# Kernel optimization log

Measured on AMD Instinct MI355X. Metric: run time of the kernel, lower is better.

The kernel has to match this reference:

```python
import jax, jax.numpy as jnp
import numpy as np

N_NODES = 50000
N_EDGES = 500000
IN_DIM = 128
HIDDEN = 32
HEADS = 8
OUT_DIM = HIDDEN * HEADS  # 256
NEG_SLOPE = 0.2


def setup_inputs() -> dict:
    key = jax.random.key(0)
    ks = jax.random.split(key, 10)
    s = lambda fan: 1.0 / np.sqrt(fan)
    x = jax.random.normal(ks[0], (N_NODES, IN_DIM), dtype=jnp.float32)
    edge_index = jax.random.randint(ks[1], (2, N_EDGES), 0, N_NODES, dtype=jnp.int32)
    W1 = jax.random.normal(ks[2], (IN_DIM, HEADS * HIDDEN), jnp.float32) * s(IN_DIM)
    a_src1 = jax.random.normal(ks[3], (HEADS, HIDDEN), jnp.float32) * s(HIDDEN)
    a_dst1 = jax.random.normal(ks[4], (HEADS, HIDDEN), jnp.float32) * s(HIDDEN)
    b1 = jnp.zeros((HEADS * HIDDEN,), jnp.float32)
    W2 = jax.random.normal(ks[5], (OUT_DIM, OUT_DIM), jnp.float32) * s(OUT_DIM)
    a_src2 = jax.random.normal(ks[6], (1, OUT_DIM), jnp.float32) * s(OUT_DIM)
    a_dst2 = jax.random.normal(ks[7], (1, OUT_DIM), jnp.float32) * s(OUT_DIM)
    b2 = jnp.zeros((OUT_DIM,), jnp.float32)
    return {"x": x, "edge_index": edge_index, "W1": W1, "a_src1": a_src1,
            "a_dst1": a_dst1, "b1": b1, "W2": W2, "a_src2": a_src2,
            "a_dst2": a_dst2, "b2": b2}


def _gat_layer(x, src, dst, W, a_src, a_dst, b, heads, ch, concat):
    N = x.shape[0]
    h = (x @ W).reshape(N, heads, ch)                      # [N,H,C]
    e_src = jnp.sum(h * a_src[None], axis=-1)              # [N,H]
    e_dst = jnp.sum(h * a_dst[None], axis=-1)              # [N,H]
    e = jax.nn.leaky_relu(e_src[src] + e_dst[dst], NEG_SLOPE)  # [E,H]
    # softmax over incoming edges of each destination node
    m = jax.ops.segment_max(e, dst, num_segments=N)        # [N,H]
    e = jnp.exp(e - m[dst])
    denom = jax.ops.segment_sum(e, dst, num_segments=N)    # [N,H]
    alpha = e / (denom[dst] + 1e-16)                       # [E,H]
    msg = h[src] * alpha[:, :, None]                       # [E,H,C]
    out = jax.ops.segment_sum(msg, dst, num_segments=N)    # [N,H,C]
    out = out.reshape(N, heads * ch) if concat else out.mean(axis=1)
    return out + b


def reference(x, edge_index, W1, a_src1, a_dst1, b1, W2, a_src2, a_dst2, b2):
    N = x.shape[0]
    # add self loops (PyG GATConv default)
    loops = jnp.arange(N, dtype=edge_index.dtype)
    src = jnp.concatenate([edge_index[0], loops])
    dst = jnp.concatenate([edge_index[1], loops])
    # dropout is identity in eval mode
    h = _gat_layer(x, src, dst, W1, a_src1, a_dst1, b1, HEADS, HIDDEN, True)
    h = jax.nn.elu(h)
    out = _gat_layer(h, src, dst, W2, a_src2, a_dst2, b2, 1, OUT_DIM, False)
    return out
```

## Files before the change

### kernel.cpp

```cpp
#include <hip/hip_runtime.h>
#include <math.h>

#define N_NODES 50000
#define E_ORIG  500000
#define E_TOT   550000
#define NB      196
#define AGG_GB  1563

typedef _Float16 half8  __attribute__((ext_vector_type(8)));
typedef _Float16 half4  __attribute__((ext_vector_type(4)));
typedef float    v4f    __attribute__((ext_vector_type(4)));
typedef int      int4u  __attribute__((ext_vector_type(4), aligned(4)));

__global__ void k_prepw(const float* __restrict__ W1, const float* __restrict__ W2,
                        const float* __restrict__ as2, const float* __restrict__ ad2,
                        const int* __restrict__ ei,
                        _Float16* __restrict__ w1t, _Float16* __restrict__ w2t,
                        float* __restrict__ vs2, float* __restrict__ vd2,
                        int* __restrict__ deg) {
    int i = blockIdx.x * blockDim.x + threadIdx.x;
    if (i < E_TOT) {
        int d = (i < E_ORIG) ? ei[E_ORIG + i] : (i - E_ORIG);
        atomicAdd(&deg[d], 1);
        return;
    }
    int j = i - E_TOT;
    if (j < 128 * 256) {
        int k = j >> 8, c = j & 255;
        w1t[(size_t)c * 128 + k] = (_Float16)W1[j];
        return;
    }
    j -= 128 * 256;
    if (j < 256 * 256) {
        int k = j >> 8, c = j & 255;
        w2t[(size_t)c * 256 + k] = (_Float16)W2[j];
        return;
    }
    j -= 256 * 256;
    if (j < 256) {
        float s = 0.f, d = 0.f;
        for (int c = 0; c < 256; c++) {
            float w = W2[(size_t)j * 256 + c];
            s += w * as2[c];
            d += w * ad2[c];
        }
        vs2[j] = s;
        vd2[j] = d;
    }
}

__global__ __launch_bounds__(256) void k_blocksum(const int* __restrict__ deg,
                                                  int* __restrict__ bsum) {
    int t = threadIdx.x;
    int i = blockIdx.x * 256 + t;
    int v = (i < N_NODES) ? deg[i] : 0;
#pragma unroll
    for (int mk = 1; mk < 64; mk <<= 1) v += __shfl_xor(v, mk, 64);
    __shared__ int ws[4];
    if ((t & 63) == 0) ws[t >> 6] = v;
    __syncthreads();
    if (t == 0) bsum[blockIdx.x] = ws[0] + ws[1] + ws[2] + ws[3];
}

__global__ __launch_bounds__(256) void k_scanbsum(const int* __restrict__ bsum,
                                                  int* __restrict__ boff) {
    __shared__ int s[256];
    int t = threadIdx.x;
    int v = (t < NB) ? bsum[t] : 0;
    s[t] = v;
    __syncthreads();
    for (int o = 1; o < 256; o <<= 1) {
        int x = (t >= o) ? s[t - o] : 0;
        __syncthreads();
        s[t] += x;
        __syncthreads();
    }
    if (t <= NB) boff[t] = (t == 0) ? 0 : s[t - 1];
}

__global__ __launch_bounds__(256) void k_offsets(const int* __restrict__ deg,
                                                 const int* __restrict__ boff,
                                                 int* __restrict__ offsets,
                                                 int* __restrict__ cur) {
    __shared__ int s[256];
    int t = threadIdx.x;
    int i = blockIdx.x * 256 + t;
    int v = (i < N_NODES) ? deg[i] : 0;
    s[t] = v;
    __syncthreads();
    for (int o = 1; o < 256; o <<= 1) {
        int x = (t >= o) ? s[t - o] : 0;
        __syncthreads();
        s[t] += x;
        __syncthreads();
    }
    int off = boff[blockIdx.x] + s[t] - v;
    if (i <= N_NODES) {
        offsets[i] = off;
        if (i < N_NODES) cur[i] = off;
    }
}

__global__ void k_scatter(const int* __restrict__ ei, int* __restrict__ cur,
                          int* __restrict__ csr_src) {
    int e = blockIdx.x * blockDim.x + threadIdx.x;
    if (e >= E_TOT) return;
    int s, d;
    if (e < E_ORIG) { s = ei[e]; d = ei[E_ORIG + e]; }
    else            { s = e - E_ORIG; d = s; }
    int slot = atomicAdd(&cur[d], 1);
    csr_src[slot] = s;
}

__global__ __launch_bounds__(256) void k_gemm1(
    const float* __restrict__ X, const _Float16* __restrict__ Bt,
    const float* __restrict__ a_s, const float* __restrict__ a_d,
    _Float16* __restrict__ H, float* __restrict__ es, float* __restrict__ ed) {
    int t = threadIdx.x, w = t >> 6, lane = t & 63;
    int quad = lane >> 4, l16 = lane & 15;
    int row0 = blockIdx.x * 32;
    int colbase = w * 64;

    v4f acc[2][4];
#pragma unroll
    for (int i = 0; i < 2; i++)
#pragma unroll
        for (int j = 0; j < 4; j++) acc[i][j] = (v4f){0.f, 0.f, 0.f, 0.f};

    int r0 = row0 + l16;      if (r0 >= N_NODES) r0 = N_NODES - 1;
    int r1 = row0 + 16 + l16; if (r1 >= N_NODES) r1 = N_NODES - 1;
    const float4* a0p = (const float4*)(X + (size_t)r0 * 128) + quad * 2;
    const float4* a1p = (const float4*)(X + (size_t)r1 * 128) + quad * 2;
    const half8* bp[4];
#pragma unroll
    for (int ct = 0; ct < 4; ct++)
        bp[ct] = (const half8*)(Bt + (size_t)(colbase + ct * 16 + l16) * 128 + quad * 8);

#pragma unroll
    for (int kc = 0; kc < 4; kc++) {
        float4 f0 = a0p[kc * 8], f1 = a0p[kc * 8 + 1];
        float4 f2 = a1p[kc * 8], f3 = a1p[kc * 8 + 1];
        half8 av0 = (half8){(_Float16)f0.x, (_Float16)f0.y, (_Float16)f0.z, (_Float16)f0.w,
                            (_Float16)f1.x, (_Float16)f1.y, (_Float16)f1.z, (_Float16)f1.w};
        half8 av1 = (half8){(_Float16)f2.x, (_Float16)f2.y, (_Float16)f2.z, (_Float16)f2.w,
                            (_Float16)f3.x, (_Float16)f3.y, (_Float16)f3.z, (_Float16)f3.w};
#pragma unroll
        for (int ct = 0; ct < 4; ct++) {
            half8 bv = bp[ct][kc * 4];
            acc[0][ct] = __builtin_amdgcn_mfma_f32_16x16x32_f16(av0, bv, acc[0][ct], 0, 0, 0);
            acc[1][ct] = __builtin_amdgcn_mfma_f32_16x16x32_f16(av1, bv, acc[1][ct], 0, 0, 0);
        }
    }

    float asv[4], adv[4];
#pragma unroll
    for (int ct = 0; ct < 4; ct++) {
        asv[ct] = a_s[colbase + ct * 16 + l16];
        adv[ct] = a_d[colbase + ct * 16 + l16];
    }
#pragma unroll
    for (int rt = 0; rt < 2; rt++) {
#pragma unroll
        for (int hp = 0; hp < 2; hp++) {
#pragma unroll
            for (int reg = 0; reg < 4; reg++) {
                float ps = acc[rt][2 * hp][reg] * asv[2 * hp] +
                           acc[rt][2 * hp + 1][reg] * asv[2 * hp + 1];
                float pd = acc[rt][2 * hp][reg] * adv[2 * hp] +
                           acc[rt][2 * hp + 1][reg] * adv[2 * hp + 1];
#pragma unroll
                for (int mk = 1; mk < 16; mk <<= 1) {
                    ps += __shfl_xor(ps, mk, 64);
                    pd += __shfl_xor(pd, mk, 64);
                }
                if (l16 == 0) {
                    int row = row0 + rt * 16 + quad * 4 + reg;
                    if (row < N_NODES) {
                        int head = w * 2 + hp;
                        es[(size_t)head * N_NODES + row] = ps;
                        ed[(size_t)head * N_NODES + row] = pd;
                    }
                }
            }
        }
    }

    __shared__ _Float16 SH[16][264];
#pragma unroll
    for (int rt = 0; rt < 2; rt++) {
        if (rt) __syncthreads();
#pragma unroll
        for (int ct = 0; ct < 4; ct++)
#pragma unroll
            for (int reg = 0; reg < 4; reg++)
                SH[quad * 4 + reg][colbase + ct * 16 + l16] = (_Float16)acc[rt][ct][reg];
        __syncthreads();
#pragma unroll
        for (int j = 0; j < 2; j++) {
            int c = j * 256 + t;
            int row = c >> 5, col8 = c & 31;
            int gr = row0 + rt * 16 + row;
            if (gr < N_NODES) {
                int head = col8 >> 2, sub = col8 & 3;
                *(half8*)(H + ((size_t)head * N_NODES + gr) * 32 + sub * 8) =
                    *(const half8*)&SH[row][col8 * 8];
            }
        }
    }
}

__global__ __launch_bounds__(256) void k_gemm2(
    const _Float16* __restrict__ A, const _Float16* __restrict__ Bt,
    const float* __restrict__ bias, float* __restrict__ OUT) {
    int t = threadIdx.x, w = t >> 6, lane = t & 63;
    int quad = lane >> 4, l16 = lane & 15;
    int row0 = blockIdx.x * 32;
    int colbase = w * 64;

    v4f acc[2][4];
#pragma unroll
    for (int i = 0; i < 2; i++)
#pragma unroll
        for (int j = 0; j < 4; j++) acc[i][j] = (v4f){0.f, 0.f, 0.f, 0.f};

    int r0 = row0 + l16;      if (r0 >= N_NODES) r0 = N_NODES - 1;
    int r1 = row0 + 16 + l16; if (r1 >= N_NODES) r1 = N_NODES - 1;
    const half8* a0 = (const half8*)(A + (size_t)r0 * 256 + quad * 8);
    const half8* a1 = (const half8*)(A + (size_t)r1 * 256 + quad * 8);
    const half8* bp[4];
#pragma unroll
    for (int ct = 0; ct < 4; ct++)
        bp[ct] = (const half8*)(Bt + (size_t)(colbase + ct * 16 + l16) * 256 + quad * 8);

#pragma unroll
    for (int kc = 0; kc < 8; kc++) {
        half8 av0 = a0[kc * 4];
        half8 av1 = a1[kc * 4];
#pragma unroll
        for (int ct = 0; ct < 4; ct++) {
            half8 bv = bp[ct][kc * 4];
            acc[0][ct] = __builtin_amdgcn_mfma_f32_16x16x32_f16(av0, bv, acc[0][ct], 0, 0, 0);
            acc[1][ct] = __builtin_amdgcn_mfma_f32_16x16x32_f16(av1, bv, acc[1][ct], 0, 0, 0);
        }
    }

    __shared__ float SF[16][260];
#pragma unroll
    for (int rt = 0; rt < 2; rt++) {
        if (rt) __syncthreads();
#pragma unroll
        for (int ct = 0; ct < 4; ct++)
#pragma unroll
            for (int reg = 0; reg < 4; reg++)
                SF[quad * 4 + reg][colbase + ct * 16 + l16] = acc[rt][ct][reg];
        __syncthreads();
#pragma unroll
        for (int j = 0; j < 4; j++) {
            int c = j * 256 + t;
            int row = c >> 6, c4 = c & 63;
            int gr = row0 + rt * 16 + row;
            if (gr < N_NODES) {
                float4 v = *(const float4*)&SF[row][c4 * 4];
                float4 bb = ((const float4*)bias)[c4];
                float4 o = make_float4(v.x + bb.x, v.y + bb.y, v.z + bb.z, v.w + bb.w);
                *(float4*)(OUT + (size_t)gr * 256 + c4 * 4) = o;
            }
        }
    }
}

__global__ __launch_bounds__(256) void k_agg1(
    const _Float16* __restrict__ Hs, const float* __restrict__ esh,
    const float* __restrict__ edh, const int* __restrict__ offsets,
    const int* __restrict__ csr_src, const float* __restrict__ b1,
    const float* __restrict__ vs2, const float* __restrict__ vd2,
    _Float16* __restrict__ out1s, float* __restrict__ es2,
    float* __restrict__ ed2) {
    int t = threadIdx.x, w = t >> 6, lane = t & 63;
    int h  = blockIdx.x & 7;
    int gb = blockIdx.x >> 3;
    int g  = lane >> 3;
    int c4 = lane & 7;
    int nn = gb * 32 + w * 8 + g;
    bool valid = nn < N_NODES;
    int n = valid ? nn : N_NODES - 1;

    int beg = offsets[n];
    int deg = offsets[n + 1] - beg;
    float edn = edh[(size_t)h * N_NODES + n];

    const _Float16* __restrict__ Hb  = Hs + (size_t)h * N_NODES * 32;
    const float* __restrict__    esb = esh + (size_t)h * N_NODES;
    const int* __restrict__      sb  = csr_src + beg;
    int bpbase = (lane & 56) << 2;

    float a0 = 0.f, a1 = 0.f, a2 = 0.f, a3 = 0.f, den = 0.f;
    for (int base = 0; base < deg; base += 8) {
        int4u sv0 = *(const int4u*)(sb + base);
        int4u sv1 = *(const int4u*)(sb + base + 4);
        int s_mine = sb[base + c4];
        float l = esb[s_mine] + edn;
        l = fmaxf(l, 0.2f * l);
        float wm = (base + c4 < deg) ? __expf(l) : 0.f;
        den += wm;
        int wmi = __float_as_int(wm);
        half4 hv[8];
        hv[0] = *(const half4*)(Hb + (size_t)sv0[0] * 32 + c4 * 4);
        hv[1] = *(const half4*)(Hb + (size_t)sv0[1] * 32 + c4 * 4);
        hv[2] = *(const half4*)(Hb + (size_t)sv0[2] * 32 + c4 * 4);
        hv[3] = *(const half4*)(Hb + (size_t)sv0[3] * 32 + c4 * 4);
        hv[4] = *(const half4*)(Hb + (size_t)sv1[0] * 32 + c4 * 4);
        hv[5] = *(const half4*)(Hb + (size_t)sv1[1] * 32 + c4 * 4);
        hv[6] = *(const half4*)(Hb + (size_t)sv1[2] * 32 + c4 * 4);
        hv[7] = *(const half4*)(Hb + (size_t)sv1[3] * 32 + c4 * 4);
#pragma unroll
        for (int j = 0; j < 8; j++) {
            float wj = __int_as_float(
                __builtin_amdgcn_ds_bpermute(bpbase + 4 * j, wmi));
            a0 += wj * (float)hv[j][0]; a1 += wj * (float)hv[j][1];
            a2 += wj * (float)hv[j][2]; a3 += wj * (float)hv[j][3];
        }
    }
#pragma unroll
    for (int mk = 1; mk < 8; mk <<= 1) den += __shfl_xor(den, mk, 64);

    float r = 1.f / (den + 1e-16f);
    int c = h * 32 + c4 * 4;
    float4 bb = *(const float4*)(b1 + c);
    float o0 = a0 * r + bb.x, o1 = a1 * r + bb.y;
    float o2 = a2 * r + bb.z, o3 = a3 * r + bb.w;
    o0 = o0 > 0.f ? o0 : __expf(o0) - 1.f;
    o1 = o1 > 0.f ? o1 : __expf(o1) - 1.f;
    o2 = o2 > 0.f ? o2 : __expf(o2) - 1.f;
    o3 = o3 > 0.f ? o3 : __expf(o3) - 1.f;
    *(half4*)(out1s + ((size_t)h * N_NODES + n) * 32 + c4 * 4) =
        (half4){(_Float16)o0, (_Float16)o1, (_Float16)o2, (_Float16)o3};

    float4 vs = *(const float4*)(vs2 + c);
    float4 vd = *(const float4*)(vd2 + c);
    float ps = o0 * vs.x + o1 * vs.y + o2 * vs.z + o3 * vs.w;
    float pd = o0 * vd.x + o1 * vd.y + o2 * vd.z + o3 * vd.w;
#pragma unroll
    for (int mk = 1; mk < 8; mk <<= 1) {
        ps += __shfl_xor(ps, mk, 64);
        pd += __shfl_xor(pd, mk, 64);
    }
    if (c4 == 0 && valid) {
        atomicAdd(&es2[n], ps);
        atomicAdd(&ed2[n], pd);
    }
}

__global__ __launch_bounds__(256) void k_agg2(
    const _Float16* __restrict__ O1s, const float* __restrict__ es2,
    const float* __restrict__ ed2, const int* __restrict__ offsets,
    const int* __restrict__ csr_src, _Float16* __restrict__ xagg) {
    int t = threadIdx.x, w = t >> 6, lane = t & 63;
    int h  = blockIdx.x & 7;
    int gb = blockIdx.x >> 3;
    int g  = lane >> 3;
    int c4 = lane & 7;
    int nn = gb * 32 + w * 8 + g;
    bool valid = nn < N_NODES;
    int n = valid ? nn : N_NODES - 1;

    int beg = offsets[n];
    int deg = offsets[n + 1] - beg;
    float edn = ed2[n];

    const _Float16* __restrict__ Ob = O1s + (size_t)h * N_NODES * 32;
    const int* __restrict__     sb  = csr_src + beg;
    int bpbase = (lane & 56) << 2;

    float a0 = 0.f, a1 = 0.f, a2 = 0.f, a3 = 0.f, den = 0.f;
    for (int base = 0; base < deg; base += 8) {
        int4u sv0 = *(const int4u*)(sb + base);
        int4u sv1 = *(const int4u*)(sb + base + 4);
        int s_mine = sb[base + c4];
        float l = es2[s_mine] + edn;
        l = fmaxf(l, 0.2f * l);
        float wm = (base + c4 < deg) ? __expf(l) : 0.f;
        den += wm;
        int wmi = __float_as_int(wm);
        half4 hv[8];
        hv[0] = *(const half4*)(Ob + (size_t)sv0[0] * 32 + c4 * 4);
        hv[1] = *(const half4*)(Ob + (size_t)sv0[1] * 32 + c4 * 4);
        hv[2] = *(const half4*)(Ob + (size_t)sv0[2] * 32 + c4 * 4);
        hv[3] = *(const half4*)(Ob + (size_t)sv0[3] * 32 + c4 * 4);
        hv[4] = *(const half4*)(Ob + (size_t)sv1[0] * 32 + c4 * 4);
        hv[5] = *(const half4*)(Ob + (size_t)sv1[1] * 32 + c4 * 4);
        hv[6] = *(const half4*)(Ob + (size_t)sv1[2] * 32 + c4 * 4);
        hv[7] = *(const half4*)(Ob + (size_t)sv1[3] * 32 + c4 * 4);
#pragma unroll
        for (int j = 0; j < 8; j++) {
            float wj = __int_as_float(
                __builtin_amdgcn_ds_bpermute(bpbase + 4 * j, wmi));
            a0 += wj * (float)hv[j][0]; a1 += wj * (float)hv[j][1];
            a2 += wj * (float)hv[j][2]; a3 += wj * (float)hv[j][3];
        }
    }
#pragma unroll
    for (int mk = 1; mk < 8; mk <<= 1) den += __shfl_xor(den, mk, 64);

    float r = 1.f / (den + 1e-16f);
    *(half4*)(xagg + (size_t)n * 256 + h * 32 + c4 * 4) =
        (half4){(_Float16)(a0 * r), (_Float16)(a1 * r),
                (_Float16)(a2 * r), (_Float16)(a3 * r)};
}

extern "C" void kernel_launch(void* const* d_in, const int* in_sizes, int n_in,
                              void* d_out, int out_size, void* d_ws, size_t ws_size,
                              hipStream_t stream) {
    const float* x   = (const float*)d_in[0];
    const int*   ei  = (const int*)d_in[1];
    const float* W1  = (const float*)d_in[2];
    const float* as1 = (const float*)d_in[3];
    const float* ad1 = (const float*)d_in[4];
    const float* b1  = (const float*)d_in[5];
    const float* W2  = (const float*)d_in[6];
    const float* as2 = (const float*)d_in[7];
    const float* ad2 = (const float*)d_in[8];
    const float* b2  = (const float*)d_in[9];
    float* out = (float*)d_out;

    char* ws = (char*)d_ws;
    size_t off = 0;
    auto alloc = [&](size_t bytes) {
        void* p = ws + off;
        off = (off + bytes + 255) & ~(size_t)255;
        return p;
    };
    _Float16* h1h     = (_Float16*)alloc((size_t)N_NODES * 256 * 2);
    _Float16* out1h   = (_Float16*)alloc((size_t)N_NODES * 256 * 2);
    _Float16* xagg    = (_Float16*)alloc((size_t)N_NODES * 256 * 2);
    _Float16* w1t     = (_Float16*)alloc((size_t)128 * 256 * 2);
    _Float16* w2t     = (_Float16*)alloc((size_t)256 * 256 * 2);
    float*    es1     = (float*)alloc((size_t)N_NODES * 8 * 4);
    float*    ed1     = (float*)alloc((size_t)N_NODES * 8 * 4);
    float*    es2     = (float*)alloc((size_t)N_NODES * 4);
    float*    ed2     = (float*)alloc((size_t)N_NODES * 4);
    float*    vs2     = (float*)alloc(256 * 4);
    float*    vd2     = (float*)alloc(256 * 4);
    int*      deg     = (int*)alloc((size_t)N_NODES * 4);
    int*      offsets = (int*)alloc((size_t)(N_NODES + 1) * 4);
    int*      cur     = (int*)alloc((size_t)N_NODES * 4);
    int*      csr_src = (int*)alloc((size_t)(E_TOT + 8) * 4);
    int*      bsum    = (int*)alloc((size_t)NB * 4);
    int*      boff    = (int*)alloc((size_t)(NB + 1) * 4);

    const int TB = 256;
    int gridE = (E_TOT + TB - 1) / TB;
    int gridG = (N_NODES + 31) / 32;
    int gridA = AGG_GB * 8;

    hipMemsetAsync(deg, 0, (size_t)N_NODES * 4, stream);
    hipMemsetAsync(es2, 0, (size_t)N_NODES * 4, stream);
    hipMemsetAsync(ed2, 0, (size_t)N_NODES * 4, stream);
    hipMemsetAsync(csr_src + E_TOT, 0, 8 * 4, stream);
    int prepN = E_TOT + 128 * 256 + 256 * 256 + 256;
    k_prepw<<<(prepN + TB - 1) / TB, TB, 0, stream>>>(W1, W2, as2, ad2, ei,
                                                      w1t, w2t, vs2, vd2, deg);
    k_blocksum<<<NB, TB, 0, stream>>>(deg, bsum);
    k_scanbsum<<<1, TB, 0, stream>>>(bsum, boff);
    k_offsets<<<NB, TB, 0, stream>>>(deg, boff, offsets, cur);
    k_scatter<<<gridE, TB, 0, stream>>>(ei, cur, csr_src);

    k_gemm1<<<gridG, TB, 0, stream>>>(x, w1t, as1, ad1, h1h, es1, ed1);
    k_agg1<<<gridA, TB, 0, stream>>>(h1h, es1, ed1, offsets, csr_src, b1,
                                     vs2, vd2, out1h, es2, ed2);

    k_agg2<<<gridA, TB, 0, stream>>>(out1h, es2, ed2, offsets, csr_src, xagg);
    k_gemm2<<<gridG, TB, 0, stream>>>(xagg, w2t, b2, out);
}
```

Baseline: 371.2 us.

## Sort nodes by degree and use 4-lane groups with half8 gathers in aggregation

Adds a counting sort of nodes by in-degree (histogram, scan, rank) to build a permutation. The aggregation kernels walk that permutation, so nodes with similar degree share a wavefront and divergence is reduced. Each node now gets 4 lanes loading half8 instead of 8 lanes loading half4, processing 4 edges per iteration and doubling the nodes per wave. The cost is three extra small kernel launches, an extra perm load, and less coalesced output writes because neighbouring lanes now handle scattered nodes.

```diff
diff --git a/kernel.cpp b/kernel.cpp
--- a/kernel.cpp
+++ b/kernel.cpp
@@ -5,7 +5,7 @@
 #define E_ORIG  500000
 #define E_TOT   550000
 #define NB      196
-#define AGG_GB  1563
+#define AGG_GB  782
 
 typedef _Float16 half8  __attribute__((ext_vector_type(8)));
 typedef _Float16 half4  __attribute__((ext_vector_type(4)));
@@ -112,6 +112,39 @@
     csr_src[slot] = s;
 }
 
+__global__ __launch_bounds__(256) void k_hist(const int* __restrict__ deg,
+                                              int* __restrict__ hist) {
+    int i = blockIdx.x * 256 + threadIdx.x;
+    if (i < N_NODES) {
+        int b = deg[i]; if (b > 63) b = 63;
+        atomicAdd(&hist[b], 1);
+    }
+}
+
+__global__ __launch_bounds__(64) void k_scanhist(const int* __restrict__ hist,
+                                                 int* __restrict__ hcur) {
+    int t = threadIdx.x;
+    int v = hist[t];
+    int inc = v;
+#pragma unroll
+    for (int o = 1; o < 64; o <<= 1) {
+        int x = __shfl_up(inc, o, 64);
+        if (t >= o) inc += x;
+    }
+    hcur[t] = inc - v;
+}
+
+__global__ __launch_bounds__(256) void k_rank(const int* __restrict__ deg,
+                                              int* __restrict__ hcur,
+                                              int* __restrict__ perm) {
+    int i = blockIdx.x * 256 + threadIdx.x;
+    if (i < N_NODES) {
+        int b = deg[i]; if (b > 63) b = 63;
+        int r = atomicAdd(&hcur[b], 1);
+        perm[r] = i;
+    }
+}
+
 __global__ __launch_bounds__(256) void k_gemm1(
     const float* __restrict__ X, const _Float16* __restrict__ Bt,
     const float* __restrict__ a_s, const float* __restrict__ a_d,
@@ -272,18 +305,19 @@
 __global__ __launch_bounds__(256) void k_agg1(
     const _Float16* __restrict__ Hs, const float* __restrict__ esh,
     const float* __restrict__ edh, const int* __restrict__ offsets,
-    const int* __restrict__ csr_src, const float* __restrict__ b1,
-    const float* __restrict__ vs2, const float* __restrict__ vd2,
-    _Float16* __restrict__ out1s, float* __restrict__ es2,
-    float* __restrict__ ed2) {
+    const int* __restrict__ csr_src, const int* __restrict__ perm,
+    const float* __restrict__ b1, const float* __restrict__ vs2,
+    const float* __restrict__ vd2, _Float16* __restrict__ out1s,
+    float* __restrict__ es2, float* __restrict__ ed2) {
     int t = threadIdx.x, w = t >> 6, lane = t & 63;
     int h  = blockIdx.x & 7;
     int gb = blockIdx.x >> 3;
-    int g  = lane >> 3;
-    int c4 = lane & 7;
-    int nn = gb * 32 + w * 8 + g;
+    int g  = lane >> 2;
+    int l3 = lane & 3;
+    int nn = gb * 64 + w * 16 + g;
     bool valid = nn < N_NODES;
-    int n = valid ? nn : N_NODES - 1;
+    int rank = valid ? nn : N_NODES - 1;
+    int n = perm[rank];
 
     int beg = offsets[n];
     int deg = offsets[n + 1] - beg;
@@ -292,60 +326,68 @@
     const _Float16* __restrict__ Hb  = Hs + (size_t)h * N_NODES * 32;
     const float* __restrict__    esb = esh + (size_t)h * N_NODES;
     const int* __restrict__      sb  = csr_src + beg;
-    int bpbase = (lane & 56) << 2;
-
-    float a0 = 0.f, a1 = 0.f, a2 = 0.f, a3 = 0.f, den = 0.f;
-    for (int base = 0; base < deg; base += 8) {
-        int4u sv0 = *(const int4u*)(sb + base);
-        int4u sv1 = *(const int4u*)(sb + base + 4);
-        int s_mine = sb[base + c4];
-        float l = esb[s_mine] + edn;
+    int bp0 = (lane & 60) << 2;
+
+    float a[8] = {0.f, 0.f, 0.f, 0.f, 0.f, 0.f, 0.f, 0.f};
+    float den = 0.f;
+    for (int base = 0; base < deg; base += 4) {
+        int4u sv = *(const int4u*)(sb + base);
+        int sm = sv[0];
+        sm = (l3 == 1) ? sv[1] : sm;
+        sm = (l3 == 2) ? sv[2] : sm;
+        sm = (l3 == 3) ? sv[3] : sm;
+        float l = esb[sm] + edn;
         l = fmaxf(l, 0.2f * l);
-        float wm = (base + c4 < deg) ? __expf(l) : 0.f;
+        float wm = (base + l3 < deg) ? __expf(l) : 0.f;
         den += wm;
         int wmi = __float_as_int(wm);
-        half4 hv[8];
-        hv[0] = *(const half4*)(Hb + (size_t)sv0[0] * 32 + c4 * 4);
-        hv[1] = *(const half4*)(Hb + (size_t)sv0[1] * 32 + c4 * 4);
-        hv[2] = *(const half4*)(Hb + (size_t)sv0[2] * 32 + c4 * 4);
-        hv[3] = *(const half4*)(Hb + (size_t)sv0[3] * 32 + c4 * 4);
-        hv[4] = *(const half4*)(Hb + (size_t)sv1[0] * 32 + c4 * 4);
-        hv[5] = *(const half4*)(Hb + (size_t)sv1[1] * 32 + c4 * 4);
-        hv[6] = *(const half4*)(Hb + (size_t)sv1[2] * 32 + c4 * 4);
-        hv[7] = *(const half4*)(Hb + (size_t)sv1[3] * 32 + c4 * 4);
-#pragma unroll
-        for (int j = 0; j < 8; j++) {
-            float wj = __int_as_float(
-                __builtin_amdgcn_ds_bpermute(bpbase + 4 * j, wmi));
-            a0 += wj * (float)hv[j][0]; a1 += wj * (float)hv[j][1];
-            a2 += wj * (float)hv[j][2]; a3 += wj * (float)hv[j][3];
-        }
-    }
-#pragma unroll
-    for (int mk = 1; mk < 8; mk <<= 1) den += __shfl_xor(den, mk, 64);
+        half8 hv0 = *(const half8*)(Hb + (size_t)sv[0] * 32 + l3 * 8);
+        half8 hv1 = *(const half8*)(Hb + (size_t)sv[1] * 32 + l3 * 8);
+        half8 hv2 = *(const half8*)(Hb + (size_t)sv[2] * 32 + l3 * 8);
+        half8 hv3 = *(const half8*)(Hb + (size_t)sv[3] * 32 + l3 * 8);
+        float w0 = __int_as_float(__builtin_amdgcn_ds_bpermute(bp0,      wmi));
+        float w1 = __int_as_float(__builtin_amdgcn_ds_bpermute(bp0 + 4,  wmi));
+        float w2 = __int_as_float(__builtin_amdgcn_ds_bpermute(bp0 + 8,  wmi));
+        float w3 = __int_as_float(__builtin_amdgcn_ds_bpermute(bp0 + 12, wmi));
+#pragma unroll
+        for (int k = 0; k < 8; k++) {
+            a[k] += w0 * (float)hv0[k];
+            a[k] += w1 * (float)hv1[k];
+            a[k] += w2 * (float)hv2[k];
+            a[k] += w3 * (float)hv3[k];
+        }
+    }
+    den += __shfl_xor(den, 1, 64);
+    den += __shfl_xor(den, 2, 64);
 
     float r = 1.f / (den + 1e-16f);
-    int c = h * 32 + c4 * 4;
-    float4 bb = *(const float4*)(b1 + c);
-    float o0 = a0 * r + bb.x, o1 = a1 * r + bb.y;
-    float o2 = a2 * r + bb.z, o3 = a3 * r + bb.w;
-    o0 = o0 > 0.f ? o0 : __expf(o0) - 1.f;
-    o1 = o1 > 0.f ? o1 : __expf(o1) - 1.f;
-    o2 = o2 > 0.f ? o2 : __expf(o2) - 1.f;
-    o3 = o3 > 0.f ? o3 : __expf(o3) - 1.f;
-    *(half4*)(out1s + ((size_t)h * N_NODES + n) * 32 + c4 * 4) =
-        (half4){(_Float16)o0, (_Float16)o1, (_Float16)o2, (_Float16)o3};
-
-    float4 vs = *(const float4*)(vs2 + c);
-    float4 vd = *(const float4*)(vd2 + c);
-    float ps = o0 * vs.x + o1 * vs.y + o2 * vs.z + o3 * vs.w;
-    float pd = o0 * vd.x + o1 * vd.y + o2 * vd.z + o3 * vd.w;
-#pragma unroll
-    for (int mk = 1; mk < 8; mk <<= 1) {
-        ps += __shfl_xor(ps, mk, 64);
-        pd += __shfl_xor(pd, mk, 64);
-    }
-    if (c4 == 0 && valid) {
+    int c = h * 32 + l3 * 8;
+    float4 b0 = *(const float4*)(b1 + c);
+    float4 b4 = *(const float4*)(b1 + c + 4);
+    float o[8];
+    o[0] = a[0] * r + b0.x; o[1] = a[1] * r + b0.y;
+    o[2] = a[2] * r + b0.z; o[3] = a[3] * r + b0.w;
+    o[4] = a[4] * r + b4.x; o[5] = a[5] * r + b4.y;
+    o[6] = a[6] * r + b4.z; o[7] = a[7] * r + b4.w;
+    half8 ov;
+#pragma unroll
+    for (int k = 0; k < 8; k++) {
+        o[k] = o[k] > 0.f ? o[k] : __expf(o[k]) - 1.f;
+        ov[k] = (_Float16)o[k];
+    }
+    *(half8*)(out1s + ((size_t)h * N_NODES + n) * 32 + l3 * 8) = ov;
+
+    float4 vsa = *(const float4*)(vs2 + c);
+    float4 vsb = *(const float4*)(vs2 + c + 4);
+    float4 vda = *(const float4*)(vd2 + c);
+    float4 vdb = *(const float4*)(vd2 + c + 4);
+    float ps = o[0] * vsa.x + o[1] * vsa.y + o[2] * vsa.z + o[3] * vsa.w +
+               o[4] * vsb.x + o[5] * vsb.y + o[6] * vsb.z + o[7] * vsb.w;
+    float pd = o[0] * vda.x + o[1] * vda.y + o[2] * vda.z + o[3] * vda.w +
+               o[4] * vdb.x + o[5] * vdb.y + o[6] * vdb.z + o[7] * vdb.w;
+    ps += __shfl_xor(ps, 1, 64); ps += __shfl_xor(ps, 2, 64);
+    pd += __shfl_xor(pd, 1, 64); pd += __shfl_xor(pd, 2, 64);
+    if (l3 == 0 && valid) {
         atomicAdd(&es2[n], ps);
         atomicAdd(&ed2[n], pd);
     }
@@ -354,15 +396,17 @@
 __global__ __launch_bounds__(256) void k_agg2(
     const _Float16* __restrict__ O1s, const float* __restrict__ es2,
     const float* __restrict__ ed2, const int* __restrict__ offsets,
-    const int* __restrict__ csr_src, _Float16* __restrict__ xagg) {
+    const int* __restrict__ csr_src, const int* __restrict__ perm,
+    _Float16* __restrict__ xagg) {
     int t = threadIdx.x, w = t >> 6, lane = t & 63;
     int h  = blockIdx.x & 7;
     int gb = blockIdx.x >> 3;
-    int g  = lane >> 3;
-    int c4 = lane & 7;
-    int nn = gb * 32 + w * 8 + g;
+    int g  = lane >> 2;
+    int l3 = lane & 3;
+    int nn = gb * 64 + w * 16 + g;
     bool valid = nn < N_NODES;
-    int n = valid ? nn : N_NODES - 1;
+    int rank = valid ? nn : N_NODES - 1;
+    int n = perm[rank];
 
     int beg = offsets[n];
     int deg = offsets[n + 1] - beg;
@@ -370,42 +414,45 @@
 
     const _Float16* __restrict__ Ob = O1s + (size_t)h * N_NODES * 32;
     const int* __restrict__     sb  = csr_src + beg;
-    int bpbase = (lane & 56) << 2;
-
-    float a0 = 0.f, a1 = 0.f, a2 = 0.f, a3 = 0.f, den = 0.f;
-    for (int base = 0; base < deg; base += 8) {
-        int4u sv0 = *(const int4u*)(sb + base);
-        int4u sv1 = *(const int4u*)(sb + base + 4);
-        int s_mine = sb[base + c4];
-        float l = es2[s_mine] + edn;
+    int bp0 = (lane & 60) << 2;
+
+    float a[8] = {0.f, 0.f, 0.f, 0.f, 0.f, 0.f, 0.f, 0.f};
+    float den = 0.f;
+    for (int base = 0; base < deg; base += 4) {
+        int4u sv = *(const int4u*)(sb + base);
+        int sm = sv[0];
+        sm = (l3 == 1) ? sv[1] : sm;
+        sm = (l3 == 2) ? sv[2] : sm;
+        sm = (l3 == 3) ? sv[3] : sm;
+        float l = es2[sm] + edn;
         l = fmaxf(l, 0.2f * l);
-        float wm = (base + c4 < deg) ? __expf(l) : 0.f;
+        float wm = (base + l3 < deg) ? __expf(l) : 0.f;
         den += wm;
         int wmi = __float_as_int(wm);
-        half4 hv[8];
-        hv[0] = *(const half4*)(Ob + (size_t)sv0[0] * 32 + c4 * 4);
-        hv[1] = *(const half4*)(Ob + (size_t)sv0[1] * 32 + c4 * 4);
-        hv[2] = *(const half4*)(Ob + (size_t)sv0[2] * 32 + c4 * 4);
-        hv[3] = *(const half4*)(Ob + (size_t)sv0[3] * 32 + c4 * 4);
-        hv[4] = *(const half4*)(Ob + (size_t)sv1[0] * 32 + c4 * 4);
-        hv[5] = *(const half4*)(Ob + (size_t)sv1[1] * 32 + c4 * 4);
-        hv[6] = *(const half4*)(Ob + (size_t)sv1[2] * 32 + c4 * 4);
-        hv[7] = *(const half4*)(Ob + (size_t)sv1[3] * 32 + c4 * 4);
-#pragma unroll
-        for (int j = 0; j < 8; j++) {
-            float wj = __int_as_float(
-                __builtin_amdgcn_ds_bpermute(bpbase + 4 * j, wmi));
-            a0 += wj * (float)hv[j][0]; a1 += wj * (float)hv[j][1];
-            a2 += wj * (float)hv[j][2]; a3 += wj * (float)hv[j][3];
-        }
-    }
-#pragma unroll
-    for (int mk = 1; mk < 8; mk <<= 1) den += __shfl_xor(den, mk, 64);
+        half8 hv0 = *(const half8*)(Ob + (size_t)sv[0] * 32 + l3 * 8);
+        half8 hv1 = *(const half8*)(Ob + (size_t)sv[1] * 32 + l3 * 8);
+        half8 hv2 = *(const half8*)(Ob + (size_t)sv[2] * 32 + l3 * 8);
+        half8 hv3 = *(const half8*)(Ob + (size_t)sv[3] * 32 + l3 * 8);
+        float w0 = __int_as_float(__builtin_amdgcn_ds_bpermute(bp0,      wmi));
+        float w1 = __int_as_float(__builtin_amdgcn_ds_bpermute(bp0 + 4,  wmi));
+        float w2 = __int_as_float(__builtin_amdgcn_ds_bpermute(bp0 + 8,  wmi));
+        float w3 = __int_as_float(__builtin_amdgcn_ds_bpermute(bp0 + 12, wmi));
+#pragma unroll
+        for (int k = 0; k < 8; k++) {
+            a[k] += w0 * (float)hv0[k];
+            a[k] += w1 * (float)hv1[k];
+            a[k] += w2 * (float)hv2[k];
+            a[k] += w3 * (float)hv3[k];
+        }
+    }
+    den += __shfl_xor(den, 1, 64);
+    den += __shfl_xor(den, 2, 64);
 
     float r = 1.f / (den + 1e-16f);
-    *(half4*)(xagg + (size_t)n * 256 + h * 32 + c4 * 4) =
-        (half4){(_Float16)(a0 * r), (_Float16)(a1 * r),
-                (_Float16)(a2 * r), (_Float16)(a3 * r)};
+    half8 ov;
+#pragma unroll
+    for (int k = 0; k < 8; k++) ov[k] = (_Float16)(a[k] * r);
+    *(half8*)(xagg + (size_t)n * 256 + h * 32 + l3 * 8) = ov;
 }
 
 extern "C" void kernel_launch(void* const* d_in, const int* in_sizes, int n_in,
@@ -445,6 +492,9 @@
     int*      offsets = (int*)alloc((size_t)(N_NODES + 1) * 4);
     int*      cur     = (int*)alloc((size_t)N_NODES * 4);
     int*      csr_src = (int*)alloc((size_t)(E_TOT + 8) * 4);
+    int*      perm    = (int*)alloc((size_t)N_NODES * 4);
+    int*      hist    = (int*)alloc(64 * 4);
+    int*      hcur    = (int*)alloc(64 * 4);
     int*      bsum    = (int*)alloc((size_t)NB * 4);
     int*      boff    = (int*)alloc((size_t)(NB + 1) * 4);
 
@@ -456,19 +506,24 @@
     hipMemsetAsync(deg, 0, (size_t)N_NODES * 4, stream);
     hipMemsetAsync(es2, 0, (size_t)N_NODES * 4, stream);
     hipMemsetAsync(ed2, 0, (size_t)N_NODES * 4, stream);
+    hipMemsetAsync(hist, 0, 64 * 4, stream);
     hipMemsetAsync(csr_src + E_TOT, 0, 8 * 4, stream);
     int prepN = E_TOT + 128 * 256 + 256 * 256 + 256;
     k_prepw<<<(prepN + TB - 1) / TB, TB, 0, stream>>>(W1, W2, as2, ad2, ei,
                                                       w1t, w2t, vs2, vd2, deg);
+    k_hist<<<NB, TB, 0, stream>>>(deg, hist);
+    k_scanhist<<<1, 64, 0, stream>>>(hist, hcur);
+    k_rank<<<NB, TB, 0, stream>>>(deg, hcur, perm);
     k_blocksum<<<NB, TB, 0, stream>>>(deg, bsum);
     k_scanbsum<<<1, TB, 0, stream>>>(bsum, boff);
     k_offsets<<<NB, TB, 0, stream>>>(deg, boff, offsets, cur);
     k_scatter<<<gridE, TB, 0, stream>>>(ei, cur, csr_src);
 
     k_gemm1<<<gridG, TB, 0, stream>>>(x, w1t, as1, ad1, h1h, es1, ed1);
-    k_agg1<<<gridA, TB, 0, stream>>>(h1h, es1, ed1, offsets, csr_src, b1,
-                                     vs2, vd2, out1h, es2, ed2);
-
-    k_agg2<<<gridA, TB, 0, stream>>>(out1h, es2, ed2, offsets, csr_src, xagg);
+    k_agg1<<<gridA, TB, 0, stream>>>(h1h, es1, ed1, offsets, csr_src, perm,
+                                     b1, vs2, vd2, out1h, es2, ed2);
+
+    k_agg2<<<gridA, TB, 0, stream>>>(out1h, es2, ed2, offsets, csr_src, perm,
+                                     xagg);
     k_gemm2<<<gridG, TB, 0, stream>>>(xagg, w2t, b2, out);
 }
```

Result: slower. 718.7 us (+93.6%).
